# Optimization experiments

Measured on AMD Instinct MI355X. Metric: run time of the kernel, lower is better.

Reference implementation:

```python
import jax, jax.numpy as jnp
import numpy as np

N_NODES = 50000
D_IN = 128
D_OUT = 64
N_ETYPES = 3
E_PER_ETYPE = 500000
P_ETYPE = 0.5  # self.p[etype] init value for every etype


def setup_inputs() -> dict:
    key = jax.random.key(0)
    k1, k2, k3, k4 = jax.random.split(key, 4)
    feat = jax.random.normal(k1, (N_NODES, D_IN), dtype=jnp.float32)
    W = jax.random.normal(k2, (D_IN, D_OUT), dtype=jnp.float32) * 0.05
    b = jax.random.normal(k3, (D_OUT,), dtype=jnp.float32) * 0.05
    # edge_index[e] = (src, dst) for etype e
    edge_index = jax.random.randint(k4, (N_ETYPES, 2, E_PER_ETYPE), 0, N_NODES, dtype=jnp.int64)
    return {"feat": feat, "W": W, "b": b, "edge_index": edge_index}


def reference(feat, W, b, edge_index):
    N = feat.shape[0]

    def agg_one_etype(ei):
        src, dst = ei[0], ei[1]
        # scatter-mean of src features onto dst nodes (dgl copy_u + mean)
        msg_sum = jax.ops.segment_sum(feat[src], dst, num_segments=N)          # [N, D]
        cnt = jax.ops.segment_sum(jnp.ones(src.shape, feat.dtype), dst, num_segments=N)
        hr = msg_sum / jnp.maximum(cnt, 1.0)[:, None]  # zero-in-degree nodes -> 0
        return jnp.tanh(hr)  # per-etype activation

    hr_all = jax.vmap(agg_one_etype)(edge_index)        # [n_etypes, N, D]
    h_homo = jnp.sum(hr_all * P_ETYPE, axis=0) + feat   # weighted sum + residual
    h_homo = jnp.tanh(h_homo)
    return h_homo @ W + b                               # final linear
```

## Files before the change

### kernel.cpp

```cpp
#include <hip/hip_runtime.h>
#include <hip/hip_bf16.h>

#define N_NODES 50000
#define D_IN 128
#define D_OUT 64
#define N_ETYPES 3
#define E_PER_ETYPE 500000
#define N_EDGES (N_ETYPES * E_PER_ETYPE)
#define CAP1 16
#define CAP2 30
#define DMAX (CAP1 + CAP2)
#define ZROW N_NODES
#define NB_FEAT ((N_NODES * D_IN / 4) / 256)
#define NB_W ((D_IN * D_OUT) / 256)
#define NZINT4 ((N_ETYPES * N_NODES + 16) / 4)
#define NB_ZCNT ((NZINT4 + 255) / 256)
#define CHUNK_EDGES 2048
#define N_CHUNKS ((N_EDGES + CHUNK_EDGES - 1) / CHUNK_EDGES)
#define NSLICE 8
#define SLICE_N 6250
#define QCAP 196608
#define NBLK_PER_SLICE 64

typedef __attribute__((ext_vector_type(8))) short short8;
typedef __attribute__((ext_vector_type(4))) float f32x4;

static __device__ __forceinline__ unsigned short f2bf(float f) {
    unsigned int x = __float_as_uint(f);
    unsigned int lsb = (x >> 16) & 1u;
    x += 0x7fffu + lsb;
    return (unsigned short)(x >> 16);
}

static __device__ __forceinline__ float fast_tanh(float x) {
    float e = __expf(2.0f * x);
    return 1.0f - 2.0f * __builtin_amdgcn_rcpf(e + 1.0f);
}

static __device__ __forceinline__ short8 as_s8(uint4 u) {
    union { uint4 u; short8 s; } cv; cv.u = u; return cv.s;
}

static __device__ __forceinline__ void accum8(float* ax, uint4 p) {
    ax[0] += __uint_as_float(p.x << 16);
    ax[1] += __uint_as_float(p.x & 0xffff0000u);
    ax[2] += __uint_as_float(p.y << 16);
    ax[3] += __uint_as_float(p.y & 0xffff0000u);
    ax[4] += __uint_as_float(p.z << 16);
    ax[5] += __uint_as_float(p.z & 0xffff0000u);
    ax[6] += __uint_as_float(p.w << 16);
    ax[7] += __uint_as_float(p.w & 0xffff0000u);
}

static __device__ __forceinline__ float2 rs_reduce(const float* ax, int sub) {
    bool hi = (sub & 1);
    float k0_ = hi ? ax[4] : ax[0], s0_ = hi ? ax[0] : ax[4];
    float k1_ = hi ? ax[5] : ax[1], s1_ = hi ? ax[1] : ax[5];
    float k2_ = hi ? ax[6] : ax[2], s2_ = hi ? ax[2] : ax[6];
    float k3_ = hi ? ax[7] : ax[3], s3_ = hi ? ax[3] : ax[7];
    float h0 = k0_ + __shfl_xor(s0_, 16);
    float h1 = k1_ + __shfl_xor(s1_, 16);
    float h2 = k2_ + __shfl_xor(s2_, 16);
    float h3 = k3_ + __shfl_xor(s3_, 16);
    bool hi2 = (sub & 2);
    float ka = hi2 ? h2 : h0, sa = hi2 ? h0 : h2;
    float kb = hi2 ? h3 : h1, sb = hi2 ? h1 : h3;
    float2 v;
    v.x = ka + __shfl_xor(sa, 32);
    v.y = kb + __shfl_xor(sb, 32);
    return v;
}

__global__ __launch_bounds__(256) void convert_kernel(
    const float* __restrict__ feat,
    unsigned short* __restrict__ featbf,
    const float* __restrict__ W,
    unsigned short* __restrict__ wtbf,
    int* __restrict__ cnt)
{
    int b = blockIdx.x;
    if (b < NB_FEAT) {
        int i = b * 256 + threadIdx.x;
        const float4* f4 = (const float4*)feat;
        float4 v = f4[i];
        ushort4 o;
        o.x = f2bf(v.x); o.y = f2bf(v.y); o.z = f2bf(v.z); o.w = f2bf(v.w);
        ((ushort4*)featbf)[i] = o;
    } else if (b < NB_FEAT + NB_W) {
        int i = (b - NB_FEAT) * 256 + threadIdx.x;
        int n = i >> 7;
        int k = i & 127;
        wtbf[i] = f2bf(W[k * D_OUT + n]);
    } else if (b == NB_FEAT + NB_W) {
        if (threadIdx.x < 64)
            ((unsigned int*)(featbf + (size_t)N_NODES * D_IN))[threadIdx.x] = 0;
    } else {
        int i = (b - NB_FEAT - NB_W - 1) * 256 + threadIdx.x;
        if (i < NZINT4) {
            int4 z; z.x = 0; z.y = 0; z.z = 0; z.w = 0;
            ((int4*)cnt)[i] = z;
        }
    }
}

__global__ __launch_bounds__(256) void partition_kernel(
    const int* __restrict__ edge_index,
    unsigned int* __restrict__ queue,
    int* __restrict__ qcnt)
{
    __shared__ int lcnt[NSLICE];
    __shared__ int lbase[NSLICE];
    int tid = threadIdx.x;
    if (tid < NSLICE) lcnt[tid] = 0;
    __syncthreads();

    int e0 = blockIdx.x * CHUNK_EDGES + tid;
    unsigned int rec[CHUNK_EDGES / 256];
    int sl[CHUNK_EDGES / 256], pos[CHUNK_EDGES / 256];
    #pragma unroll
    for (int k = 0; k < CHUNK_EDGES / 256; k++) {
        int e = e0 + k * 256;
        sl[k] = -1;
        if (e < N_EDGES) {
            int t  = e / E_PER_ETYPE;
            int ei = e - t * E_PER_ETYPE;
            const int* base = edge_index + (long long)t * 2 * E_PER_ETYPE;
            int src = __builtin_nontemporal_load(base + ei);
            int dst = __builtin_nontemporal_load(base + E_PER_ETYPE + ei);
            int s = (int)(((unsigned long long)(unsigned)dst * 687195ull) >> 32);
            int ldst = dst - s * SLICE_N;
            rec[k] = (unsigned)src | ((unsigned)ldst << 16) | ((unsigned)t << 29);
            sl[k]  = s;
            pos[k] = atomicAdd(&lcnt[s], 1);
        }
    }
    __syncthreads();
    if (tid < NSLICE) lbase[tid] = atomicAdd(&qcnt[tid], lcnt[tid]);
    __syncthreads();
    #pragma unroll
    for (int k = 0; k < CHUNK_EDGES / 256; k++) {
        if (sl[k] >= 0) {
            int p = lbase[sl[k]] + pos[k];
            if (p < QCAP)
                queue[sl[k] * QCAP + p] = rec[k];
        }
    }
}

__global__ __launch_bounds__(256) void binfill_kernel(
    const unsigned int* __restrict__ queue,
    const int* __restrict__ qcnt,
    unsigned short* __restrict__ bucket1,
    unsigned short* __restrict__ spill,
    int* __restrict__ cnt)
{
    int slice = blockIdx.x & 7;
    int blk   = blockIdx.x >> 3;
    int total = qcnt[slice];
    const unsigned int* q = queue + slice * QCAP;
    int sbase = slice * SLICE_N;
    for (int i = blk * 256 + threadIdx.x; i < total; i += NBLK_PER_SLICE * 256) {
        unsigned int r = __builtin_nontemporal_load(q + i);
        int src  = r & 0xFFFF;
        int ldst = (r >> 16) & 0x1FFF;
        int t    = r >> 29;
        int cell = t * N_NODES + sbase + ldst;
        int p = atomicAdd(cnt + cell, 1);
        if (p < CAP1)
            bucket1[cell * CAP1 + p] = (unsigned short)src;
        else if (p < DMAX)
            spill[cell * CAP2 + (p - CAP1)] = (unsigned short)src;
    }
}

__global__ __launch_bounds__(256) void fill_kernel(
    const int* __restrict__ edge_index,
    unsigned short* __restrict__ bucket1,
    unsigned short* __restrict__ spill,
    int* __restrict__ cnt)
{
    int slice = blockIdx.x & 7;
    int chunk = blockIdx.x >> 3;
    int e0 = chunk * CHUNK_EDGES + threadIdx.x;
    #pragma unroll
    for (int k = 0; k < CHUNK_EDGES / 256; k++) {
        int e = e0 + k * 256;
        if (e < N_EDGES) {
            int t  = e / E_PER_ETYPE;
            int ei = e - t * E_PER_ETYPE;
            const int* base = edge_index + (long long)t * 2 * E_PER_ETYPE;
            int dst = base[E_PER_ETYPE + ei];
            int s = (int)(((unsigned long long)(unsigned)dst * 687195ull) >> 32);
            if (s == slice) {
                int src = base[ei];
                int cell = t * N_NODES + dst;
                int pos = atomicAdd(cnt + cell, 1);
                if (pos < CAP1)
                    bucket1[cell * CAP1 + pos] = (unsigned short)src;
                else if (pos < CAP1 + CAP2)
                    spill[cell * CAP2 + (pos - CAP1)] = (unsigned short)src;
            }
        }
    }
}

__global__ __launch_bounds__(512) void gather_linear_kernel(
    const float* __restrict__ feat,
    const unsigned short* __restrict__ featbf,
    const unsigned short* __restrict__ wtbf,
    const float* __restrict__ bg,
    const unsigned short* __restrict__ bucket1,
    const unsigned short* __restrict__ spill,
    const int* __restrict__ cnt,
    float* __restrict__ out)
{
    __shared__ unsigned short hsb[16 * 128];

    int tid = threadIdx.x;
    int wave = tid >> 6;
    int lane = tid & 63;
    int sub  = lane >> 4;
    int sl   = lane & 15;
    int n0 = blockIdx.x * 16 + wave * 2;
    int n1 = n0 + 1;

    int degA[N_ETYPES], degB[N_ETYPES], idxA[N_ETYPES], idxB[N_ETYPES];
    #pragma unroll
    for (int t = 0; t < N_ETYPES; t++) {
        int cell = t * N_NODES + n0;
        int2 dg = *(const int2*)(cnt + cell);
        int la = 0, lb = 0;
        if (lane < CAP1) {
            la = bucket1[cell * CAP1 + lane];
            lb = bucket1[(cell + 1) * CAP1 + lane];
        } else if (lane < DMAX) {
            if (dg.x > CAP1) la = spill[cell * CAP2 + (lane - CAP1)];
            if (dg.y > CAP1) lb = spill[(cell + 1) * CAP2 + (lane - CAP1)];
        }
        int ca = dg.x < DMAX ? dg.x : DMAX;
        int cb = dg.y < DMAX ? dg.y : DMAX;
        idxA[t] = (lane < ca) ? la : ZROW;
        idxB[t] = (lane < cb) ? lb : ZROW;
        degA[t] = dg.x; degB[t] = dg.y;
    }

    int k0 = ((sub & 1) << 2) | (sub & 2);
    int p2 = 4 * sl + (k0 >> 1);
    float2 fA = ((const float2*)feat)[n0 * 64 + p2];
    float2 fB = ((const float2*)feat)[n1 * 64 + p2];

    const uint4* fb4 = (const uint4*)featbf;
    float s0A = 0.0f, s1A = 0.0f, s0B = 0.0f, s1B = 0.0f;

    #pragma unroll
    for (int t = 0; t < N_ETYPES; t++) {
        int da = degA[t] < DMAX ? degA[t] : DMAX;
        int db = degB[t] < DMAX ? degB[t] : DMAX;
        int dm = da > db ? da : db;
        float axA[8], axB[8];
        #pragma unroll
        for (int k = 0; k < 8; k++) { axA[k] = 0.0f; axB[k] = 0.0f; }
        for (int j = 0; j < dm; j += 8) {
            int r0 = j + sub;
            int r1 = j + 4 + sub;
            int sa0 = __shfl(idxA[t], r0);
            int sa1 = __shfl(idxA[t], r1);
            int sb0 = __shfl(idxB[t], r0);
            int sb1 = __shfl(idxB[t], r1);
            uint4 pa0 = fb4[sa0 * 16 + sl];
            uint4 pa1 = fb4[sa1 * 16 + sl];
            uint4 pb0 = fb4[sb0 * 16 + sl];
            uint4 pb1 = fb4[sb1 * 16 + sl];
            accum8(axA, pa0); accum8(axA, pa1);
            accum8(axB, pb0); accum8(axB, pb1);
        }
        float2 vA = rs_reduce(axA, sub);
        float2 vB = rs_reduce(axB, sub);
        float invA = __builtin_amdgcn_rcpf((float)(degA[t] > 0 ? degA[t] : 1));
        float invB = __builtin_amdgcn_rcpf((float)(degB[t] > 0 ? degB[t] : 1));
        s0A += fast_tanh(vA.x * invA);
        s1A += fast_tanh(vA.y * invA);
        s0B += fast_tanh(vB.x * invB);
        s1B += fast_tanh(vB.y * invB);
    }

    float hxA = fast_tanh(fA.x + 0.5f * s0A);
    float hyA = fast_tanh(fA.y + 0.5f * s1A);
    float hxB = fast_tanh(fB.x + 0.5f * s0B);
    float hyB = fast_tanh(fB.y + 0.5f * s1B);
    unsigned int hpA = (unsigned int)f2bf(hxA) | ((unsigned int)f2bf(hyA) << 16);
    unsigned int hpB = (unsigned int)f2bf(hxB) | ((unsigned int)f2bf(hyB) << 16);
    int colb = 16 * sl + 2 * k0;
    int rA = wave * 2, rB = rA + 1;
    ((unsigned int*)hsb)[(rA * 256 + (colb ^ ((rA & 7) << 4))) >> 2] = hpA;
    ((unsigned int*)hsb)[(rB * 256 + (colb ^ ((rB & 7) << 4))) >> 2] = hpB;

    uint4 b0 = {0,0,0,0}, b1 = {0,0,0,0}, b2 = {0,0,0,0}, b3 = {0,0,0,0};
    float bias = 0.0f;
    if (wave < 4) {
        int nrow = wave * 16 + sl;
        const uint4* wt4 = (const uint4*)wtbf;
        b0 = wt4[nrow * 16 +  0 + sub];
        b1 = wt4[nrow * 16 +  4 + sub];
        b2 = wt4[nrow * 16 +  8 + sub];
        b3 = wt4[nrow * 16 + 12 + sub];
        bias = bg[nrow];
    }
    __syncthreads();

    if (wave < 4) {
        int row = sl;
        int rbase = row * 256;
        int rx = (row & 7) << 4;
        const uint4* h4 = (const uint4*)hsb;
        uint4 a0 = h4[(rbase + (( 0 + sub * 16) ^ rx)) >> 4];
        uint4 a1 = h4[(rbase + (( 64 + sub * 16) ^ rx)) >> 4];
        uint4 a2 = h4[(rbase + ((128 + sub * 16) ^ rx)) >> 4];
        uint4 a3 = h4[(rbase + ((192 + sub * 16) ^ rx)) >> 4];

        f32x4 c = {bias, bias, bias, bias};
        c = __builtin_amdgcn_mfma_f32_16x16x32_bf16(as_s8(a0), as_s8(b0), c, 0, 0, 0);
        c = __builtin_amdgcn_mfma_f32_16x16x32_bf16(as_s8(a1), as_s8(b1), c, 0, 0, 0);
        c = __builtin_amdgcn_mfma_f32_16x16x32_bf16(as_s8(a2), as_s8(b2), c, 0, 0, 0);
        c = __builtin_amdgcn_mfma_f32_16x16x32_bf16(as_s8(a3), as_s8(b3), c, 0, 0, 0);

        #pragma unroll
        for (int i = 0; i < 4; i++) {
            int orow = sub * 4 + i;
            out[(blockIdx.x * 16 + orow) * 64 + wave * 16 + sl] = c[i];
        }
    }
}

extern "C" void kernel_launch(void* const* d_in, const int* in_sizes, int n_in,
                              void* d_out, int out_size, void* d_ws, size_t ws_size,
                              hipStream_t stream) {
    const float* feat = (const float*)d_in[0];
    const float* W    = (const float*)d_in[1];
    const float* b    = (const float*)d_in[2];
    const int* edge_index = (const int*)d_in[3];
    float* out = (float*)d_out;

    size_t featbf_bytes  = (size_t)(N_NODES + 1) * D_IN * sizeof(unsigned short);
    size_t bucket1_bytes = (size_t)N_ETYPES * N_NODES * CAP1 * sizeof(unsigned short);
    size_t spill_bytes   = (size_t)N_ETYPES * N_NODES * CAP2 * sizeof(unsigned short);
    size_t cnt_bytes     = (size_t)(N_ETYPES * N_NODES + 16) * sizeof(int);
    size_t wtbf_bytes    = (size_t)D_IN * D_OUT * sizeof(unsigned short);
    size_t base_bytes    = featbf_bytes + bucket1_bytes + spill_bytes + cnt_bytes + wtbf_bytes;
    size_t queue_bytes   = (size_t)NSLICE * QCAP * sizeof(unsigned int);
    if (ws_size < base_bytes)
        return;
    bool twophase = (ws_size >= base_bytes + queue_bytes);

    unsigned short* featbf  = (unsigned short*)d_ws;
    unsigned short* bucket1 = (unsigned short*)((char*)d_ws + featbf_bytes);
    unsigned short* spill   = (unsigned short*)((char*)d_ws + featbf_bytes + bucket1_bytes);
    int* cnt = (int*)((char*)d_ws + featbf_bytes + bucket1_bytes + spill_bytes);
    int* qcnt = cnt + N_ETYPES * N_NODES;
    unsigned short* wtbf = (unsigned short*)((char*)d_ws + featbf_bytes + bucket1_bytes
                                             + spill_bytes + cnt_bytes);
    unsigned int* queue = (unsigned int*)((char*)d_ws + base_bytes);

    convert_kernel<<<NB_FEAT + NB_W + 1 + NB_ZCNT, 256, 0, stream>>>(
        feat, featbf, W, wtbf, cnt);

    if (twophase) {
        partition_kernel<<<N_CHUNKS, 256, 0, stream>>>(edge_index, queue, qcnt);
        binfill_kernel<<<NSLICE * NBLK_PER_SLICE, 256, 0, stream>>>(
            queue, qcnt, bucket1, spill, cnt);
    } else {
        fill_kernel<<<N_CHUNKS * 8, 256, 0, stream>>>(edge_index, bucket1, spill, cnt);
    }

    gather_linear_kernel<<<N_NODES / 16, 512, 0, stream>>>(
        feat, featbf, wtbf, b, bucket1, spill, cnt, out);
}
```

Baseline: 216.0 us.

## Drop two-phase partition path, use single-pass fill with nontemporal loads

Removes the partition+binfill two-phase bucketing and always launches the slice-filtered fill_kernel, which now reads edge indices with nontemporal loads. The gather kernel loads counts and bucket entries nontemporally and takes the residual feature from the bf16 copy instead of fp32 feat. This cuts one kernel launch and the queue traffic, but every edge's dst is now read eight times (once per slice). The bf16 residual also slightly lowers precision.

```diff
diff --git a/kernel.cpp b/kernel.cpp
--- a/kernel.cpp
+++ b/kernel.cpp
@@ -103,6 +103,37 @@
     }
 }
 
+__global__ __launch_bounds__(256) void fill_kernel(
+    const int* __restrict__ edge_index,
+    unsigned short* __restrict__ bucket1,
+    unsigned short* __restrict__ spill,
+    int* __restrict__ cnt)
+{
+    int slice = blockIdx.x & 7;
+    int chunk = blockIdx.x >> 3;
+    int e0 = chunk * CHUNK_EDGES + threadIdx.x;
+    #pragma unroll
+    for (int k = 0; k < CHUNK_EDGES / 256; k++) {
+        int e = e0 + k * 256;
+        if (e < N_EDGES) {
+            int t  = e / E_PER_ETYPE;
+            int ei = e - t * E_PER_ETYPE;
+            const int* base = edge_index + (long long)t * 2 * E_PER_ETYPE;
+            int dst = __builtin_nontemporal_load(base + E_PER_ETYPE + ei);
+            int s = (int)(((unsigned long long)(unsigned)dst * 687195ull) >> 32);
+            if (s == slice) {
+                int src = __builtin_nontemporal_load(base + ei);
+                int cell = t * N_NODES + dst;
+                int pos = atomicAdd(cnt + cell, 1);
+                if (pos < CAP1)
+                    bucket1[cell * CAP1 + pos] = (unsigned short)src;
+                else if (pos < CAP1 + CAP2)
+                    spill[cell * CAP2 + (pos - CAP1)] = (unsigned short)src;
+            }
+        }
+    }
+}
+
 __global__ __launch_bounds__(256) void partition_kernel(
     const int* __restrict__ edge_index,
     unsigned int* __restrict__ queue,
@@ -113,7 +144,6 @@
     int tid = threadIdx.x;
     if (tid < NSLICE) lcnt[tid] = 0;
     __syncthreads();
-
     int e0 = blockIdx.x * CHUNK_EDGES + tid;
     unsigned int rec[CHUNK_EDGES / 256];
     int sl[CHUNK_EDGES / 256], pos[CHUNK_EDGES / 256];
@@ -173,37 +203,6 @@
     }
 }
 
-__global__ __launch_bounds__(256) void fill_kernel(
-    const int* __restrict__ edge_index,
-    unsigned short* __restrict__ bucket1,
-    unsigned short* __restrict__ spill,
-    int* __restrict__ cnt)
-{
-    int slice = blockIdx.x & 7;
-    int chunk = blockIdx.x >> 3;
-    int e0 = chunk * CHUNK_EDGES + threadIdx.x;
-    #pragma unroll
-    for (int k = 0; k < CHUNK_EDGES / 256; k++) {
-        int e = e0 + k * 256;
-        if (e < N_EDGES) {
-            int t  = e / E_PER_ETYPE;
-            int ei = e - t * E_PER_ETYPE;
-            const int* base = edge_index + (long long)t * 2 * E_PER_ETYPE;
-            int dst = base[E_PER_ETYPE + ei];
-            int s = (int)(((unsigned long long)(unsigned)dst * 687195ull) >> 32);
-            if (s == slice) {
-                int src = base[ei];
-                int cell = t * N_NODES + dst;
-                int pos = atomicAdd(cnt + cell, 1);
-                if (pos < CAP1)
-                    bucket1[cell * CAP1 + pos] = (unsigned short)src;
-                else if (pos < CAP1 + CAP2)
-                    spill[cell * CAP2 + (pos - CAP1)] = (unsigned short)src;
-            }
-        }
-    }
-}
-
 __global__ __launch_bounds__(512) void gather_linear_kernel(
     const float* __restrict__ feat,
     const unsigned short* __restrict__ featbf,
@@ -228,26 +227,29 @@
     #pragma unroll
     for (int t = 0; t < N_ETYPES; t++) {
         int cell = t * N_NODES + n0;
-        int2 dg = *(const int2*)(cnt + cell);
+        unsigned long long dgp = __builtin_nontemporal_load(
+            (const unsigned long long*)(cnt + cell));
+        int dgx = (int)(dgp & 0xffffffffull);
+        int dgy = (int)(dgp >> 32);
         int la = 0, lb = 0;
         if (lane < CAP1) {
-            la = bucket1[cell * CAP1 + lane];
-            lb = bucket1[(cell + 1) * CAP1 + lane];
+            la = __builtin_nontemporal_load(bucket1 + cell * CAP1 + lane);
+            lb = __builtin_nontemporal_load(bucket1 + (cell + 1) * CAP1 + lane);
         } else if (lane < DMAX) {
-            if (dg.x > CAP1) la = spill[cell * CAP2 + (lane - CAP1)];
-            if (dg.y > CAP1) lb = spill[(cell + 1) * CAP2 + (lane - CAP1)];
-        }
-        int ca = dg.x < DMAX ? dg.x : DMAX;
-        int cb = dg.y < DMAX ? dg.y : DMAX;
+            if (dgx > CAP1) la = __builtin_nontemporal_load(spill + cell * CAP2 + (lane - CAP1));
+            if (dgy > CAP1) lb = __builtin_nontemporal_load(spill + (cell + 1) * CAP2 + (lane - CAP1));
+        }
+        int ca = dgx < DMAX ? dgx : DMAX;
+        int cb = dgy < DMAX ? dgy : DMAX;
         idxA[t] = (lane < ca) ? la : ZROW;
         idxB[t] = (lane < cb) ? lb : ZROW;
-        degA[t] = dg.x; degB[t] = dg.y;
+        degA[t] = dgx; degB[t] = dgy;
     }
 
     int k0 = ((sub & 1) << 2) | (sub & 2);
     int p2 = 4 * sl + (k0 >> 1);
-    float2 fA = ((const float2*)feat)[n0 * 64 + p2];
-    float2 fB = ((const float2*)feat)[n1 * 64 + p2];
+    unsigned int rfA = ((const unsigned int*)featbf)[n0 * 64 + p2];
+    unsigned int rfB = ((const unsigned int*)featbf)[n1 * 64 + p2];
 
     const uint4* fb4 = (const uint4*)featbf;
     float s0A = 0.0f, s1A = 0.0f, s0B = 0.0f, s1B = 0.0f;
@@ -284,10 +286,14 @@
         s1B += fast_tanh(vB.y * invB);
     }
 
-    float hxA = fast_tanh(fA.x + 0.5f * s0A);
-    float hyA = fast_tanh(fA.y + 0.5f * s1A);
-    float hxB = fast_tanh(fB.x + 0.5f * s0B);
-    float hyB = fast_tanh(fB.y + 0.5f * s1B);
+    float fAx = __uint_as_float(rfA << 16);
+    float fAy = __uint_as_float(rfA & 0xffff0000u);
+    float fBx = __uint_as_float(rfB << 16);
+    float fBy = __uint_as_float(rfB & 0xffff0000u);
+    float hxA = fast_tanh(fAx + 0.5f * s0A);
+    float hyA = fast_tanh(fAy + 0.5f * s1A);
+    float hxB = fast_tanh(fBx + 0.5f * s0B);
+    float hyB = fast_tanh(fBy + 0.5f * s1B);
     unsigned int hpA = (unsigned int)f2bf(hxA) | ((unsigned int)f2bf(hyA) << 16);
     unsigned int hpB = (unsigned int)f2bf(hxB) | ((unsigned int)f2bf(hyB) << 16);
     int colb = 16 * sl + 2 * k0;
@@ -347,30 +353,20 @@
     size_t cnt_bytes     = (size_t)(N_ETYPES * N_NODES + 16) * sizeof(int);
     size_t wtbf_bytes    = (size_t)D_IN * D_OUT * sizeof(unsigned short);
     size_t base_bytes    = featbf_bytes + bucket1_bytes + spill_bytes + cnt_bytes + wtbf_bytes;
-    size_t queue_bytes   = (size_t)NSLICE * QCAP * sizeof(unsigned int);
     if (ws_size < base_bytes)
         return;
-    bool twophase = (ws_size >= base_bytes + queue_bytes);
 
     unsigned short* featbf  = (unsigned short*)d_ws;
     unsigned short* bucket1 = (unsigned short*)((char*)d_ws + featbf_bytes);
     unsigned short* spill   = (unsigned short*)((char*)d_ws + featbf_bytes + bucket1_bytes);
     int* cnt = (int*)((char*)d_ws + featbf_bytes + bucket1_bytes + spill_bytes);
-    int* qcnt = cnt + N_ETYPES * N_NODES;
     unsigned short* wtbf = (unsigned short*)((char*)d_ws + featbf_bytes + bucket1_bytes
                                              + spill_bytes + cnt_bytes);
-    unsigned int* queue = (unsigned int*)((char*)d_ws + base_bytes);
 
     convert_kernel<<<NB_FEAT + NB_W + 1 + NB_ZCNT, 256, 0, stream>>>(
         feat, featbf, W, wtbf, cnt);
 
-    if (twophase) {
-        partition_kernel<<<N_CHUNKS, 256, 0, stream>>>(edge_index, queue, qcnt);
-        binfill_kernel<<<NSLICE * NBLK_PER_SLICE, 256, 0, stream>>>(
-            queue, qcnt, bucket1, spill, cnt);
-    } else {
-        fill_kernel<<<N_CHUNKS * 8, 256, 0, stream>>>(edge_index, bucket1, spill, cnt);
-    }
+    fill_kernel<<<N_CHUNKS * 8, 256, 0, stream>>>(edge_index, bucket1, spill, cnt);
 
     gather_linear_kernel<<<N_NODES / 16, 512, 0, stream>>>(
         feat, featbf, wtbf, b, bucket1, spill, cnt, out);
```

New measurement: 210.7 us. -2.5%, faster.
